# Kernel optimization log

Measured on AMD Instinct MI355X. Metric: run time of the kernel, lower is better.

The kernel has to match this reference:

```python
import jax, jax.numpy as jnp
import numpy as np

B, C, T, F = 2, 256, 1024, 64
N, HID = 4, 64


def setup_inputs() -> dict:
    key = jax.random.key(0)
    ks = jax.random.split(key, 9)
    s = 0.02
    return {
        "x": jax.random.normal(ks[0], (B, C, T, F), dtype=jnp.float32),
        "Wq": jax.random.normal(ks[1], (N, HID, C), dtype=jnp.float32) * s,
        "bq": jnp.zeros((N, HID), dtype=jnp.float32),
        "Wk": jax.random.normal(ks[2], (N, HID, C), dtype=jnp.float32) * s,
        "bk": jnp.zeros((N, HID), dtype=jnp.float32),
        "Wv": jax.random.normal(ks[3], (N, C // N, C), dtype=jnp.float32) * s,
        "bv": jnp.zeros((N, C // N), dtype=jnp.float32),
        "Wp": jax.random.normal(ks[4], (C, C), dtype=jnp.float32) * s,
        "bp": jnp.zeros((C,), dtype=jnp.float32),
    }


def reference(x, Wq, bq, Wk, bk, Wv, bv, Wp, bp):
    b, c, t, f = x.shape
    n = Wq.shape[0]
    # conv1x1 per head then torch: cat(dim=0) -> [N*b, h, t, f]; transpose(1,2); flatten -> [N*b, t, h*f]
    def proj(W, bias):
        h = W.shape[1]
        y = jnp.einsum('bctf,nhc->nbthf', x, W) + bias[:, None, None, :, None]
        return y.reshape(n * b, t, h * f)

    Q = proj(Wq, bq)                       # [N*b, t, hid*f]
    K = proj(Wk, bk)                       # [N*b, t, hid*f]
    V = proj(Wv, bv)                       # [N*b, t, (c/N)*f]

    scale = 1.0 / jnp.sqrt(jnp.asarray(Q.shape[-1], dtype=x.dtype))
    attn = jax.nn.softmax(jnp.einsum('mte,mse->mts', Q, K) * scale, axis=2)
    Vo = jnp.einsum('mts,msd->mtd', attn, V)             # [N*b, t, c*f/N]

    # torch: reshape(b*N, t, c*f//N).transpose(1,2).view(N,b,c//N,t,f).transpose(0,1).view(b,c,t,f)
    Vo = Vo.transpose(0, 2, 1)                            # [N*b, c*f/N, t]
    Vo = Vo.reshape(n, b, c // n, t, f)
    Vo = jnp.swapaxes(Vo, 0, 1).reshape(b, c, t, f)

    out = jnp.einsum('bctf,oc->botf', Vo, Wp) + bp[None, :, None, None]
    return out + x
```

## Files before the change

### kernel.cpp

```cpp
#include <hip/hip_runtime.h>

#define DI __device__ __forceinline__

static constexpr int B_ = 2;
static constexpr int C_ = 256;
static constexpr int T_ = 1024;
static constexpr int F_ = 64;
static constexpr int M_ = 8;
static constexpr int E_ = 4096;
static constexpr float SCALE_ = 1.0f / 64.0f;

typedef __attribute__((ext_vector_type(8))) short bf16x8;
typedef __attribute__((ext_vector_type(4))) float f32x4;

DI unsigned short bf16_rne(float f) {
    unsigned int u = __float_as_uint(f);
    return (unsigned short)((u + 0x7FFFu + ((u >> 16) & 1u)) >> 16);
}
DI float bf2f(unsigned short h) { return __uint_as_float(((unsigned int)h) << 16); }
DI ushort4 pack4(float a, float b, float c, float d) {
    return make_ushort4(bf16_rne(a), bf16_rne(b), bf16_rne(c), bf16_rne(d));
}
DI float4 up4(ushort4 u) {
    return make_float4(bf2f(u.x), bf2f(u.y), bf2f(u.z), bf2f(u.w));
}

DI void gload_lds16(const unsigned short* g, unsigned short* l) {
    __builtin_amdgcn_global_load_lds(
        (const __attribute__((address_space(1))) unsigned int*)g,
        (__attribute__((address_space(3))) unsigned int*)l, 16, 0, 0);
}

DI void mfma16(f32x4& acc, bf16x8 a, bf16x8 b) {
    asm("v_mfma_f32_16x16x32_bf16 %0, %1, %2, %0" : "+v"(acc) : "v"(a), "v"(b));
}

__global__ __launch_bounds__(256) void wconv_kernel(
    const float* __restrict__ Wq, const float* __restrict__ Wk,
    const float* __restrict__ Wv, const float* __restrict__ Wp,
    const float* __restrict__ bq, const float* __restrict__ bk,
    const float* __restrict__ bv,
    unsigned short* __restrict__ Wall, unsigned short* __restrict__ Wpb,
    float* __restrict__ bias_all)
{
    const int tid = (int)threadIdx.x;
    const int bid = (int)blockIdx.x;
    if (bid < 192) {
        const int idx = (bid * 256 + tid) * 4;
        const int proj = idx >> 16, rem = idx & 65535;
        const float* src = proj == 0 ? Wq : (proj == 1 ? Wk : Wv);
        float4 v = *(const float4*)(src + rem);
        *(ushort4*)(Wall + idx) = pack4(v.x, v.y, v.z, v.w);
        const int gid = bid * 256 + tid;
        if (gid < 768) {
            float bb = gid < 256 ? bq[gid] : (gid < 512 ? bk[gid - 256] : bv[gid - 512]);
            bias_all[gid] = bb;
        }
    } else {
        const int idx = ((bid - 192) * 256 + tid) * 4;
        float4 v = *(const float4*)(Wp + idx);
        *(ushort4*)(Wpb + idx) = pack4(v.x, v.y, v.z, v.w);
    }
}

__global__ __launch_bounds__(256) void xt_kernel(
    const float* __restrict__ x, unsigned short* __restrict__ xT)
{
    const int tf0 = blockIdx.x * 64;
    const int c0  = blockIdx.y * 64;
    const int b   = blockIdx.z;
    const int tid = (int)threadIdx.x;
    __shared__ unsigned short ts[64][68];

    const float* xb = x + (size_t)(b * 256 + c0) * 65536 + tf0;
#pragma unroll
    for (int it = 0; it < 4; ++it) {
        int idx = it * 256 + tid;
        int cl = idx >> 4, tf4 = (idx & 15) * 4;
        float4 v = *(const float4*)(xb + (size_t)cl * 65536 + tf4);
        *(ushort4*)&ts[cl][tf4] = pack4(v.x, v.y, v.z, v.w);
    }
    __syncthreads();
    const int tfl = tid >> 2, c16 = (tid & 3) * 16;
    unsigned short* op = xT + ((size_t)b * 65536 + tf0 + tfl) * 256 + c0 + c16;
#pragma unroll
    for (int q = 0; q < 4; ++q) {
        int cl = c16 + q * 4;
        ushort4 v = make_ushort4(ts[cl][tfl], ts[cl+1][tfl], ts[cl+2][tfl], ts[cl+3][tfl]);
        *(ushort4*)(op + q * 4) = v;
    }
}

__global__ __launch_bounds__(256) void qkv_mfma(
    const unsigned short* __restrict__ xT, const unsigned short* __restrict__ Wall,
    const float* __restrict__ bias_all, unsigned short* __restrict__ outQ,
    int ntile_off, int nb_n, int proj_base)
{
    const int total = (int)gridDim.x;
    const int orig = (int)blockIdx.x;
    const int wgid = (orig & 7) * (total >> 3) + (orig >> 3);
    const int ntl = wgid % nb_n;
    const int rest = wgid / nb_n;
    const int b = rest >> 9, tft = rest & 511;
    const int ntile = ntile_off + ntl;
    const int tfbase = tft * 128;
    const int nbase = ntile * 128;

    const int tid = (int)threadIdx.x;
    const int wid = tid >> 6, lane = tid & 63;
    const int wr = wid >> 1, wc = wid & 1;
    const int lo16 = lane & 15, hi4 = lane >> 4;

    __shared__ unsigned short As[128 * 64];
    __shared__ unsigned short Bs[128 * 64];

    f32x4 acc[4][4] = {};

    const unsigned short* arow = xT + ((size_t)b * 65536 + tfbase) * 256;
    const unsigned short* brow = Wall + (size_t)nbase * 256;

    const int srow = lane >> 3;
    const int scol = ((lane & 7) ^ srow) * 8;

    for (int cb = 0; cb < 256; cb += 64) {
#pragma unroll
        for (int i = 0; i < 4; ++i) {
            const int rb = wid * 32 + i * 8;
            gload_lds16(arow + (size_t)(rb + srow) * 256 + cb + scol, &As[rb * 64]);
            gload_lds16(brow + (size_t)(rb + srow) * 256 + cb + scol, &Bs[rb * 64]);
        }
        __syncthreads();
#pragma unroll
        for (int kk = 0; kk < 2; ++kk) {
            const int hc = (kk * 32 + hi4 * 8) ^ ((lane & 7) << 3);
            bf16x8 a[4], bb[4];
#pragma unroll
            for (int mi = 0; mi < 4; ++mi)
                a[mi] = *(const bf16x8*)&As[(wr * 64 + mi * 16 + lo16) * 64 + hc];
#pragma unroll
            for (int nj = 0; nj < 4; ++nj)
                bb[nj] = *(const bf16x8*)&Bs[(wc * 64 + nj * 16 + lo16) * 64 + hc];
#pragma unroll
            for (int mi = 0; mi < 4; ++mi)
#pragma unroll
                for (int nj = 0; nj < 4; ++nj)
                    mfma16(acc[mi][nj], a[mi], bb[nj]);
        }
        __syncthreads();
    }

    asm volatile("s_nop 7\n\ts_nop 7" ::: "memory");
    const int tf0 = tfbase + wr * 64;
#pragma unroll
    for (int nj = 0; nj < 4; ++nj) {
        const int r_col = nbase + wc * 64 + nj * 16 + lo16;
        const int projl = (r_col >> 8) - proj_base;
        const int rr = r_col & 255;
        const int mrow = (rr >> 6) * 2 + b;
        const int h = rr & 63;
        const float bv = bias_all[r_col];
        unsigned short* dst0 = outQ + (size_t)projl * 33554432
                             + (size_t)mrow * (T_ * E_) + h * 64;
#pragma unroll
        for (int mi = 0; mi < 4; ++mi) {
            const int tf = tf0 + mi * 16 + hi4 * 4;
            const int t = tf >> 6, f = tf & 63;
            *(ushort4*)(dst0 + (size_t)t * E_ + f) =
                pack4(acc[mi][nj][0] + bv, acc[mi][nj][1] + bv,
                      acc[mi][nj][2] + bv, acc[mi][nj][3] + bv);
        }
    }
}

__global__ __launch_bounds__(256) void scores_mfma(
    const unsigned short* __restrict__ Q, const unsigned short* __restrict__ K,
    unsigned short* __restrict__ S)
{
    const int m = blockIdx.z;
    const int tbase = blockIdx.y * 128;
    const int sbase = blockIdx.x * 128;
    const int tid = (int)threadIdx.x;
    const int wid = tid >> 6, lane = tid & 63;
    const int wr = wid >> 1, wc = wid & 1;
    const int lo16 = lane & 15, hi4 = lane >> 4;

    __shared__ unsigned short As[128 * 64];
    __shared__ unsigned short Bs[128 * 64];

    f32x4 acc[4][4] = {};

    const unsigned short* qrow = Q + ((size_t)m * T_ + tbase) * E_;
    const unsigned short* krow = K + ((size_t)m * T_ + sbase) * E_;

    const int srow = lane >> 3;
    const int scol = ((lane & 7) ^ srow) * 8;

    for (int eb = 0; eb < E_; eb += 64) {
#pragma unroll
        for (int i = 0; i < 4; ++i) {
            const int rb = wid * 32 + i * 8;
            gload_lds16(qrow + (size_t)(rb + srow) * E_ + eb + scol, &As[rb * 64]);
            gload_lds16(krow + (size_t)(rb + srow) * E_ + eb + scol, &Bs[rb * 64]);
        }
        __syncthreads();
#pragma unroll
        for (int kk = 0; kk < 2; ++kk) {
            const int hc = (kk * 32 + hi4 * 8) ^ ((lane & 7) << 3);
            bf16x8 a[4], bb[4];
#pragma unroll
            for (int mi = 0; mi < 4; ++mi)
                a[mi] = *(const bf16x8*)&As[(wr * 64 + mi * 16 + lo16) * 64 + hc];
#pragma unroll
            for (int nj = 0; nj < 4; ++nj)
                bb[nj] = *(const bf16x8*)&Bs[(wc * 64 + nj * 16 + lo16) * 64 + hc];
#pragma unroll
            for (int mi = 0; mi < 4; ++mi)
#pragma unroll
                for (int nj = 0; nj < 4; ++nj)
                    mfma16(acc[mi][nj], a[mi], bb[nj]);
        }
        __syncthreads();
    }

    asm volatile("s_nop 7\n\ts_nop 7" ::: "memory");
#pragma unroll
    for (int mi = 0; mi < 4; ++mi)
#pragma unroll
        for (int r = 0; r < 4; ++r) {
            int trow = tbase + wr * 64 + mi * 16 + hi4 * 4 + r;
            unsigned short* sp = S + ((size_t)m * T_ + trow) * T_ + sbase + wc * 64 + lo16;
#pragma unroll
            for (int nj = 0; nj < 4; ++nj)
                sp[nj * 16] = bf16_rne(acc[mi][nj][r] * SCALE_);
        }
}

__global__ __launch_bounds__(256) void softmax_kernel(
    const unsigned short* __restrict__ S, unsigned short* __restrict__ A)
{
    const size_t rowoff = ((size_t)blockIdx.y * T_ + blockIdx.x) * T_;
    const int tid = (int)threadIdx.x;
    const int wid = tid >> 6, lane = tid & 63;

    __shared__ float redmx[4];
    __shared__ float redsm[4];

    float4 v = up4(*(const ushort4*)(S + rowoff + tid * 4));
    float mx = fmaxf(fmaxf(v.x, v.y), fmaxf(v.z, v.w));
#pragma unroll
    for (int off = 32; off > 0; off >>= 1) mx = fmaxf(mx, __shfl_xor(mx, off));
    if (lane == 0) redmx[wid] = mx;
    __syncthreads();
    mx = fmaxf(fmaxf(redmx[0], redmx[1]), fmaxf(redmx[2], redmx[3]));

    float e0 = __expf(v.x - mx), e1 = __expf(v.y - mx);
    float e2 = __expf(v.z - mx), e3 = __expf(v.w - mx);
    float sm = (e0 + e1) + (e2 + e3);
#pragma unroll
    for (int off = 32; off > 0; off >>= 1) sm += __shfl_xor(sm, off);
    if (lane == 0) redsm[wid] = sm;
    __syncthreads();
    sm = (redsm[0] + redsm[1]) + (redsm[2] + redsm[3]);
    float inv = 1.0f / sm;
    *(ushort4*)(A + rowoff + tid * 4) = pack4(e0 * inv, e1 * inv, e2 * inv, e3 * inv);
}

__global__ __launch_bounds__(256) void vt_kernel(
    const unsigned short* __restrict__ V, unsigned short* __restrict__ Vt)
{
    const int m = blockIdx.z;
    const int d0 = blockIdx.x * 64;
    const int s0 = blockIdx.y * 64;
    const int tid = (int)threadIdx.x;
    __shared__ unsigned short ts[64][68];

    const unsigned short* vp = V + (size_t)m * T_ * E_;
#pragma unroll
    for (int it = 0; it < 4; ++it) {
        int idx = it * 256 + tid;
        int sl = idx >> 4, d4 = (idx & 15) * 4;
        *(ushort4*)&ts[sl][d4] = *(const ushort4*)&vp[(size_t)(s0 + sl) * E_ + d0 + d4];
    }
    __syncthreads();
    unsigned short* op = Vt + (size_t)m * E_ * T_;
    const int dl = tid >> 2, s16 = (tid & 3) * 16;
#pragma unroll
    for (int q = 0; q < 4; ++q) {
        int s4 = s16 + q * 4;
        ushort4 v = make_ushort4(ts[s4][dl], ts[s4+1][dl], ts[s4+2][dl], ts[s4+3][dl]);
        *(ushort4*)&op[(size_t)(d0 + dl) * T_ + s0 + s4] = v;
    }
}

__global__ __launch_bounds__(256) void pv_mfma(
    const unsigned short* __restrict__ A, const unsigned short* __restrict__ Vt,
    unsigned short* __restrict__ G)
{
    const int m = blockIdx.z;
    const int nh = m >> 1, b = m & 1;
    const int tbase = blockIdx.y * 128;
    const int dbase = blockIdx.x * 128;
    const int tid = (int)threadIdx.x;
    const int wid = tid >> 6, lane = tid & 63;
    const int wr = wid >> 1, wc = wid & 1;
    const int lo16 = lane & 15, hi4 = lane >> 4;

    __shared__ unsigned short As[128 * 64];
    __shared__ unsigned short Bs[128 * 64];

    f32x4 acc[4][4] = {};

    const unsigned short* arow = A  + ((size_t)m * T_ + tbase) * T_;
    const unsigned short* vrow = Vt + (size_t)m * E_ * T_ + (size_t)dbase * T_;

    const int srow = lane >> 3;
    const int scol = ((lane & 7) ^ srow) * 8;

    for (int sb = 0; sb < T_; sb += 64) {
#pragma unroll
        for (int i = 0; i < 4; ++i) {
            const int rb = wid * 32 + i * 8;
            gload_lds16(arow + (size_t)(rb + srow) * T_ + sb + scol, &As[rb * 64]);
            gload_lds16(vrow + (size_t)(rb + srow) * T_ + sb + scol, &Bs[rb * 64]);
        }
        __syncthreads();
#pragma unroll
        for (int kk = 0; kk < 2; ++kk) {
            const int hc = (kk * 32 + hi4 * 8) ^ ((lane & 7) << 3);
            bf16x8 a[4], bb[4];
#pragma unroll
            for (int mi = 0; mi < 4; ++mi)
                a[mi] = *(const bf16x8*)&As[(wr * 64 + mi * 16 + lo16) * 64 + hc];
#pragma unroll
            for (int nj = 0; nj < 4; ++nj)
                bb[nj] = *(const bf16x8*)&Bs[(wc * 64 + nj * 16 + lo16) * 64 + hc];
#pragma unroll
            for (int mi = 0; mi < 4; ++mi)
#pragma unroll
                for (int nj = 0; nj < 4; ++nj)
                    mfma16(acc[mi][nj], a[mi], bb[nj]);
        }
        __syncthreads();
    }

    asm volatile("s_nop 7\n\ts_nop 7" ::: "memory");
    const int cb   = nh * 64 + (dbase >> 6) + wc;
    const int t2lo = (tbase >> 6) + wr;
#pragma unroll
    for (int mi = 0; mi < 4; ++mi) {
        const int tl = mi * 16 + hi4 * 4;
#pragma unroll
        for (int nj = 0; nj < 4; ++nj) {
            const int d63 = nj * 16 + lo16;
            size_t addr = (((size_t)(b * 256 + cb)) * 1024 + d63 * 16 + t2lo) * 64 + tl;
            *(ushort4*)&G[addr] = pack4(acc[mi][nj][0], acc[mi][nj][1],
                                        acc[mi][nj][2], acc[mi][nj][3]);
        }
    }
}

__global__ __launch_bounds__(256) void gt_kernel(
    const unsigned short* __restrict__ G, unsigned short* __restrict__ GT)
{
    const int tf0 = blockIdx.x * 64;
    const int c0  = blockIdx.y * 64;
    const int b   = blockIdx.z;
    const int tid = (int)threadIdx.x;
    __shared__ unsigned short ts[64][68];

    const unsigned short* gb = G + (size_t)(b * 256 + c0) * 65536 + tf0;
#pragma unroll
    for (int it = 0; it < 4; ++it) {
        int idx = it * 256 + tid;
        int cl = idx >> 4, tf4 = (idx & 15) * 4;
        *(ushort4*)&ts[cl][tf4] = *(const ushort4*)(gb + (size_t)cl * 65536 + tf4);
    }
    __syncthreads();
    const int tfl = tid >> 2, c16 = (tid & 3) * 16;
    unsigned short* op = GT + ((size_t)b * 65536 + tf0 + tfl) * 256 + c0 + c16;
#pragma unroll
    for (int q = 0; q < 4; ++q) {
        int cl = c16 + q * 4;
        ushort4 v = make_ushort4(ts[cl][tfl], ts[cl+1][tfl], ts[cl+2][tfl], ts[cl+3][tfl]);
        *(ushort4*)(op + q * 4) = v;
    }
}

__global__ __launch_bounds__(256) void outproj_mfma(
    const unsigned short* __restrict__ GT, const unsigned short* __restrict__ Wpb,
    const float* __restrict__ bp, const float* __restrict__ x,
    float* __restrict__ out)
{
    const int tfbase = blockIdx.x * 128;
    const int obase  = blockIdx.y * 128;
    const int b      = blockIdx.z;
    const int tid = (int)threadIdx.x;
    const int wid = tid >> 6, lane = tid & 63;
    const int wr = wid >> 1, wc = wid & 1;
    const int lo16 = lane & 15, hi4 = lane >> 4;

    __shared__ unsigned short As[128 * 64];
    __shared__ unsigned short Bs[128 * 64];

    f32x4 acc[4][4] = {};

    const unsigned short* arow = GT + ((size_t)b * 65536 + tfbase) * 256;
    const unsigned short* brow = Wpb + (size_t)obase * 256;

    const int srow = lane >> 3;
    const int scol = ((lane & 7) ^ srow) * 8;

    for (int cb = 0; cb < 256; cb += 64) {
#pragma unroll
        for (int i = 0; i < 4; ++i) {
            const int rb = wid * 32 + i * 8;
            gload_lds16(arow + (size_t)(rb + srow) * 256 + cb + scol, &As[rb * 64]);
            gload_lds16(brow + (size_t)(rb + srow) * 256 + cb + scol, &Bs[rb * 64]);
        }
        __syncthreads();
#pragma unroll
        for (int kk = 0; kk < 2; ++kk) {
            const int hc = (kk * 32 + hi4 * 8) ^ ((lane & 7) << 3);
            bf16x8 a[4], bb[4];
#pragma unroll
            for (int mi = 0; mi < 4; ++mi)
                a[mi] = *(const bf16x8*)&As[(wr * 64 + mi * 16 + lo16) * 64 + hc];
#pragma unroll
            for (int nj = 0; nj < 4; ++nj)
                bb[nj] = *(const bf16x8*)&Bs[(wc * 64 + nj * 16 + lo16) * 64 + hc];
#pragma unroll
            for (int mi = 0; mi < 4; ++mi)
#pragma unroll
                for (int nj = 0; nj < 4; ++nj)
                    mfma16(acc[mi][nj], a[mi], bb[nj]);
        }
        __syncthreads();
    }

    asm volatile("s_nop 7\n\ts_nop 7" ::: "memory");
#pragma unroll
    for (int nj = 0; nj < 4; ++nj) {
        const int o = obase + wc * 64 + nj * 16 + lo16;
        const float bias = bp[o];
        const size_t rowb = ((size_t)(b * 256 + o)) * 65536;
#pragma unroll
        for (int mi = 0; mi < 4; ++mi) {
            const int tf = tfbase + wr * 64 + mi * 16 + hi4 * 4;
            float4 xv = *(const float4*)(x + rowb + tf);
            float4 r = make_float4(acc[mi][nj][0] + bias + xv.x,
                                   acc[mi][nj][1] + bias + xv.y,
                                   acc[mi][nj][2] + bias + xv.z,
                                   acc[mi][nj][3] + bias + xv.w);
            *(float4*)(out + rowb + tf) = r;
        }
    }
}

extern "C" void kernel_launch(void* const* d_in, const int* in_sizes, int n_in,
                              void* d_out, int out_size, void* d_ws, size_t ws_size,
                              hipStream_t stream) {
    const float* x  = (const float*)d_in[0];
    const float* Wq = (const float*)d_in[1];
    const float* bq = (const float*)d_in[2];
    const float* Wk = (const float*)d_in[3];
    const float* bk = (const float*)d_in[4];
    const float* Wv = (const float*)d_in[5];
    const float* bv = (const float*)d_in[6];
    const float* Wp = (const float*)d_in[7];
    const float* bp = (const float*)d_in[8];
    float* out = (float*)d_out;

    char* ws = (char*)d_ws;
    unsigned short* Q    = (unsigned short*)(ws);
    unsigned short* K    = (unsigned short*)(ws + 67108864);
    unsigned short* xT   = (unsigned short*)(ws + 134217728);
    unsigned short* S    = (unsigned short*)(ws + 201326592);
    unsigned short* A    = (unsigned short*)(ws + 218103808);
    unsigned short* Wall = (unsigned short*)(ws + 234881024);
    float* bias_all      = (float*)(ws + 235274240);
    unsigned short* Wpb  = (unsigned short*)(ws + 235277312);
    unsigned short* V  = Q;
    unsigned short* Vt = K;
    unsigned short* G  = xT;
    unsigned short* GT = Q;

    wconv_kernel<<<256, 256, 0, stream>>>(Wq, Wk, Wv, Wp, bq, bk, bv, Wall, Wpb, bias_all);
    xt_kernel<<<dim3(1024, 4, 2), 256, 0, stream>>>(x, xT);
    qkv_mfma<<<4096, 256, 0, stream>>>(xT, Wall, bias_all, Q, 0, 4, 0);
    scores_mfma<<<dim3(8, 8, M_), 256, 0, stream>>>(Q, K, S);
    qkv_mfma<<<2048, 256, 0, stream>>>(xT, Wall, bias_all, V, 4, 2, 2);
    softmax_kernel<<<dim3(T_, M_), 256, 0, stream>>>(S, A);
    vt_kernel<<<dim3(64, 16, M_), 256, 0, stream>>>(V, Vt);
    pv_mfma<<<dim3(32, 8, M_), 256, 0, stream>>>(A, Vt, G);
    gt_kernel<<<dim3(1024, 4, 2), 256, 0, stream>>>(G, GT);
    outproj_mfma<<<dim3(512, 2, 2), 256, 0, stream>>>(GT, Wpb, bp, x, out);
}
```

Baseline: 429.3 us.

## Keep x tile resident in LDS and loop over all output column tiles

The QKV projection kernel now loads the full 128x256 activation tile into shared memory once per block, then iterates over all N-tiles of the weight matrix, streaming only the weight tiles. This removes repeated global reads of the same activation rows across separate blocks. The trade-offs are a 64KB+16KB LDS footprint per block, which limits occupancy, four times fewer blocks, and the loss of the XCD-aware block remapping.

```diff
diff --git a/kernel.cpp b/kernel.cpp
--- a/kernel.cpp
+++ b/kernel.cpp
@@ -91,83 +91,89 @@
     }
 }
 
-__global__ __launch_bounds__(256) void qkv_mfma(
+__global__ __launch_bounds__(256) void qkv_fused(
     const unsigned short* __restrict__ xT, const unsigned short* __restrict__ Wall,
     const float* __restrict__ bias_all, unsigned short* __restrict__ outQ,
     int ntile_off, int nb_n, int proj_base)
 {
-    const int total = (int)gridDim.x;
-    const int orig = (int)blockIdx.x;
-    const int wgid = (orig & 7) * (total >> 3) + (orig >> 3);
-    const int ntl = wgid % nb_n;
-    const int rest = wgid / nb_n;
-    const int b = rest >> 9, tft = rest & 511;
-    const int ntile = ntile_off + ntl;
+    const int wgid = (int)blockIdx.x;
+    const int b = wgid >> 9, tft = wgid & 511;
     const int tfbase = tft * 128;
-    const int nbase = ntile * 128;
 
     const int tid = (int)threadIdx.x;
     const int wid = tid >> 6, lane = tid & 63;
     const int wr = wid >> 1, wc = wid & 1;
     const int lo16 = lane & 15, hi4 = lane >> 4;
 
-    __shared__ unsigned short As[128 * 64];
+    __shared__ unsigned short As[4 * 128 * 64];
     __shared__ unsigned short Bs[128 * 64];
 
-    f32x4 acc[4][4] = {};
-
     const unsigned short* arow = xT + ((size_t)b * 65536 + tfbase) * 256;
-    const unsigned short* brow = Wall + (size_t)nbase * 256;
 
     const int srow = lane >> 3;
     const int scol = ((lane & 7) ^ srow) * 8;
 
-    for (int cb = 0; cb < 256; cb += 64) {
+#pragma unroll
+    for (int kc = 0; kc < 4; ++kc)
 #pragma unroll
         for (int i = 0; i < 4; ++i) {
             const int rb = wid * 32 + i * 8;
-            gload_lds16(arow + (size_t)(rb + srow) * 256 + cb + scol, &As[rb * 64]);
-            gload_lds16(brow + (size_t)(rb + srow) * 256 + cb + scol, &Bs[rb * 64]);
-        }
-        __syncthreads();
-#pragma unroll
-        for (int kk = 0; kk < 2; ++kk) {
-            const int hc = (kk * 32 + hi4 * 8) ^ ((lane & 7) << 3);
-            bf16x8 a[4], bb[4];
-#pragma unroll
-            for (int mi = 0; mi < 4; ++mi)
-                a[mi] = *(const bf16x8*)&As[(wr * 64 + mi * 16 + lo16) * 64 + hc];
-#pragma unroll
-            for (int nj = 0; nj < 4; ++nj)
-                bb[nj] = *(const bf16x8*)&Bs[(wc * 64 + nj * 16 + lo16) * 64 + hc];
-#pragma unroll
-            for (int mi = 0; mi < 4; ++mi)
+            gload_lds16(arow + (size_t)(rb + srow) * 256 + kc * 64 + scol,
+                        &As[kc * 8192 + rb * 64]);
+        }
+
+    const int tf0 = tfbase + wr * 64;
+    for (int ntl = 0; ntl < nb_n; ++ntl) {
+        const int nbase = (ntile_off + ntl) * 128;
+        const unsigned short* brow = Wall + (size_t)nbase * 256;
+        f32x4 acc[4][4] = {};
+
+        for (int kc = 0; kc < 4; ++kc) {
+#pragma unroll
+            for (int i = 0; i < 4; ++i) {
+                const int rb = wid * 32 + i * 8;
+                gload_lds16(brow + (size_t)(rb + srow) * 256 + kc * 64 + scol,
+                            &Bs[rb * 64]);
+            }
+            __syncthreads();
+#pragma unroll
+            for (int kk = 0; kk < 2; ++kk) {
+                const int hc = (kk * 32 + hi4 * 8) ^ ((lane & 7) << 3);
+                bf16x8 a[4], bb[4];
+#pragma unroll
+                for (int mi = 0; mi < 4; ++mi)
+                    a[mi] = *(const bf16x8*)&As[kc * 8192 + (wr * 64 + mi * 16 + lo16) * 64 + hc];
 #pragma unroll
                 for (int nj = 0; nj < 4; ++nj)
-                    mfma16(acc[mi][nj], a[mi], bb[nj]);
-        }
-        __syncthreads();
-    }
-
-    asm volatile("s_nop 7\n\ts_nop 7" ::: "memory");
-    const int tf0 = tfbase + wr * 64;
-#pragma unroll
-    for (int nj = 0; nj < 4; ++nj) {
-        const int r_col = nbase + wc * 64 + nj * 16 + lo16;
-        const int projl = (r_col >> 8) - proj_base;
-        const int rr = r_col & 255;
-        const int mrow = (rr >> 6) * 2 + b;
-        const int h = rr & 63;
-        const float bv = bias_all[r_col];
-        unsigned short* dst0 = outQ + (size_t)projl * 33554432
-                             + (size_t)mrow * (T_ * E_) + h * 64;
-#pragma unroll
-        for (int mi = 0; mi < 4; ++mi) {
-            const int tf = tf0 + mi * 16 + hi4 * 4;
-            const int t = tf >> 6, f = tf & 63;
-            *(ushort4*)(dst0 + (size_t)t * E_ + f) =
-                pack4(acc[mi][nj][0] + bv, acc[mi][nj][1] + bv,
-                      acc[mi][nj][2] + bv, acc[mi][nj][3] + bv);
+                    bb[nj] = *(const bf16x8*)&Bs[(wc * 64 + nj * 16 + lo16) * 64 + hc];
+#pragma unroll
+                for (int mi = 0; mi < 4; ++mi)
+#pragma unroll
+                    for (int nj = 0; nj < 4; ++nj)
+                        mfma16(acc[mi][nj], a[mi], bb[nj]);
+            }
+            __syncthreads();
+        }
+
+        asm volatile("s_nop 7\n\ts_nop 7" ::: "memory");
+#pragma unroll
+        for (int nj = 0; nj < 4; ++nj) {
+            const int r_col = nbase + wc * 64 + nj * 16 + lo16;
+            const int projl = (r_col >> 8) - proj_base;
+            const int rr = r_col & 255;
+            const int mrow = (rr >> 6) * 2 + b;
+            const int h = rr & 63;
+            const float bv = bias_all[r_col];
+            unsigned short* dst0 = outQ + (size_t)projl * 33554432
+                                 + (size_t)mrow * (T_ * E_) + h * 64;
+#pragma unroll
+            for (int mi = 0; mi < 4; ++mi) {
+                const int tf = tf0 + mi * 16 + hi4 * 4;
+                const int t = tf >> 6, f = tf & 63;
+                *(ushort4*)(dst0 + (size_t)t * E_ + f) =
+                    pack4(acc[mi][nj][0] + bv, acc[mi][nj][1] + bv,
+                          acc[mi][nj][2] + bv, acc[mi][nj][3] + bv);
+            }
         }
     }
 }
@@ -486,9 +492,9 @@
 
     wconv_kernel<<<256, 256, 0, stream>>>(Wq, Wk, Wv, Wp, bq, bk, bv, Wall, Wpb, bias_all);
     xt_kernel<<<dim3(1024, 4, 2), 256, 0, stream>>>(x, xT);
-    qkv_mfma<<<4096, 256, 0, stream>>>(xT, Wall, bias_all, Q, 0, 4, 0);
+    qkv_fused<<<1024, 256, 0, stream>>>(xT, Wall, bias_all, Q, 0, 4, 0);
     scores_mfma<<<dim3(8, 8, M_), 256, 0, stream>>>(Q, K, S);
-    qkv_mfma<<<2048, 256, 0, stream>>>(xT, Wall, bias_all, V, 4, 2, 2);
+    qkv_fused<<<1024, 256, 0, stream>>>(xT, Wall, bias_all, V, 4, 2, 2);
     softmax_kernel<<<dim3(T_, M_), 256, 0, stream>>>(S, A);
     vt_kernel<<<dim3(64, 16, M_), 256, 0, stream>>>(V, Vt);
     pv_mfma<<<dim3(32, 8, M_), 256, 0, stream>>>(A, Vt, G);
```

Result: no change. 431.7 us (+0.6%).
